# Optimization experiments

Hardware: AMD Instinct MI355X
Metric: run time of the kernel (lower is better)

The kernel has to match this reference:

```python
import jax, jax.numpy as jnp
import numpy as np

K = 3
PAD = 1
STRIDE = 1
DIL = 1


def _conv_offset(x, w, b):
    # standard 3x3 conv, NCHW
    out = jax.lax.conv_general_dilated(
        x, w, window_strides=(STRIDE, STRIDE), padding=((PAD, PAD), (PAD, PAD)),
        rhs_dilation=(DIL, DIL), dimension_numbers=('NCHW', 'OIHW', 'NCHW'))
    return out + b[None, :, None, None]


def _bilinear_sample(x, px, py):
    # x: (b,c,h,w); px,py: (b,N) absolute pixel coords; zero padding outside.
    b, c, h, w = x.shape
    x_flat = x.reshape(b, c, h * w)
    x0 = jnp.floor(px)
    y0 = jnp.floor(py)
    wx1 = px - x0
    wy1 = py - y0
    wx0 = 1.0 - wx1
    wy0 = 1.0 - wy1

    def gather(xi, yi, wt):
        valid = (xi >= 0) & (xi <= w - 1) & (yi >= 0) & (yi <= h - 1)
        xc = jnp.clip(xi, 0, w - 1).astype(jnp.int32)
        yc = jnp.clip(yi, 0, h - 1).astype(jnp.int32)
        idx = yc * w + xc  # (b,N)
        v = jax.vmap(lambda xf, i: jnp.take(xf, i, axis=1))(x_flat, idx)  # (b,c,N)
        return v * (wt * valid.astype(x.dtype))[:, None, :]

    out = gather(x0, y0, wy0 * wx0)
    out = out + gather(x0 + 1, y0, wy0 * wx1)
    out = out + gather(x0, y0 + 1, wy1 * wx0)
    out = out + gather(x0 + 1, y0 + 1, wy1 * wx1)
    return out


def setup_inputs() -> dict:
    key = jax.random.key(0)
    k1, k2, k3, k4 = jax.random.split(key, 4)
    x = jax.random.normal(k1, (8, 64, 128, 128), dtype=jnp.float32)
    # small random offset-predictor weights (repo inits to zero; random gives nonzero offsets)
    w_off = jax.random.normal(k2, (27, 64, 3, 3), dtype=jnp.float32) * 0.01
    b_off = jax.random.normal(k3, (27,), dtype=jnp.float32) * 0.01
    w_conv = jax.random.normal(k4, (64, 576), dtype=jnp.float32) / np.sqrt(3.0 * 576.0)
    return {"x": x, "w_off": w_off, "b_off": b_off, "w_conv": w_conv}


def reference(x, w_off, b_off, w_conv):
    b, c, h, w = x.shape
    out = _conv_offset(x, w_off, b_off)  # (b, 3*K*K, H, W)
    H, W = out.shape[2], out.shape[3]
    o1, o2, m = jnp.split(out, 3, axis=1)  # each (b, K*K, H, W)
    mask = jax.nn.sigmoid(m).reshape(b, 1, K, K, H, W)
    # base grid (absolute coords), per module __init__
    x_start = DIL / 2 * (K - 1) - PAD  # = 0.0 here
    y_start = DIL / 2 * (K - 1) - PAD
    x_cood = (x_start + STRIDE * jnp.arange(W)).astype(x.dtype)
    y_cood = (y_start + STRIDE * jnp.arange(H)).astype(x.dtype)
    # per-tap kernel bias, tap order is (kh, kw) row-major
    taps = (jnp.arange(K) - (K - 1) / 2) * DIL
    x_bias = jnp.tile(taps, K).astype(x.dtype)      # (K*K,)
    y_bias = jnp.repeat(taps, K).astype(x.dtype)    # (K*K,)
    px = o1 + x_cood[None, None, None, :] + x_bias[None, :, None, None]  # (b,9,H,W)
    py = o2 + y_cood[None, None, :, None] + y_bias[None, :, None, None]
    N = K * K * H * W
    y = _bilinear_sample(x, px.reshape(b, N), py.reshape(b, N))  # (b,c,N)
    y = y.reshape(b, c, K, K, H, W) * mask
    y = y.reshape(b, c * K * K, H, W)
    # 1x1 conv == channel GEMM
    return jnp.einsum('bkhw,ok->bohw', y, w_conv)
```

## Files before the change

### kernel.cpp

```cpp
#include <hip/hip_runtime.h>
#include <math.h>

#define HW_   128
#define CIN_  64
#define IMG_  (HW_ * HW_)

#define TR_    6
#define TC_    40
#define PIT_   36
#define TILEDW (TR_ * TC_ * PIT_)

typedef short    s16x8 __attribute__((ext_vector_type(8)));
typedef float    f32x4 __attribute__((ext_vector_type(4)));
typedef float    f32x2 __attribute__((ext_vector_type(2)));
typedef unsigned u32x4 __attribute__((ext_vector_type(4)));

__device__ __forceinline__ short f2bf(float f) {
  union { float f; unsigned i; } v; v.f = f;
  unsigned r = (v.i + 0x7fffu + ((v.i >> 16) & 1u)) >> 16;
  return (short)r;
}

#if defined(__has_builtin)
#if __has_builtin(__builtin_amdgcn_cvt_pk_bf16_f32)
#define HAVE_CVT_PK_BF16 1
#endif
#endif

__device__ __forceinline__ unsigned PK2(float a, float b) {
#ifdef HAVE_CVT_PK_BF16
  typedef __bf16 bf16x2_t __attribute__((ext_vector_type(2)));
  union { bf16x2_t v; unsigned u; } cv;
  cv.v = __builtin_amdgcn_cvt_pk_bf16_f32(a, b);
  return cv.u;
#else
  union { float f; unsigned u; } ua, ub; ua.f = a; ub.f = b;
  unsigned ra = ua.u + 0x7fffu + ((ua.u >> 16) & 1u);
  unsigned rb = ub.u + 0x7fffu + ((ub.u >> 16) & 1u);
  return __builtin_amdgcn_perm(rb, ra, 0x07060302u);
#endif
}

__device__ __forceinline__ f32x2 up2d(unsigned d) {
  union { unsigned u; float f; } lo, hi;
  lo.u = d << 16; hi.u = d;
  return (f32x2){lo.f, hi.f};
}


__global__ __launch_bounds__(256) void wprep(const float* __restrict__ w_off,
                                             const float* __restrict__ w_conv,
                                             short* __restrict__ wOf,
                                             short* __restrict__ wA) {
  int t = blockIdx.x * 256 + threadIdx.x;
  if (t < 36864) {
    int i = t & 7, o = (t >> 3) & 63, q = (t >> 9) & 3, ks = (t >> 11) & 1, j = t >> 12;
    int c = ks * 32 + q * 8 + i;
    wA[t] = f2bf(w_conv[o * 576 + c * 9 + j]);
  }
  if (t < 18432) {
    int i = t & 7, m = (t >> 3) & 31, q = (t >> 8) & 3, ks = (t >> 10) & 1, j = t >> 11;
    int c = ks * 32 + q * 8 + i;
    wOf[t] = (m < 27) ? f2bf(w_off[(m * 64 + c) * 9 + j]) : (short)0;
  }
}

__global__ __launch_bounds__(256)
__attribute__((amdgpu_waves_per_eu(4)))
void dfuse(const float* __restrict__ x,
           const short* __restrict__ wOf,
           const float* __restrict__ b_off,
           const short* __restrict__ wA,
           float* __restrict__ out) {
  __shared__ __align__(16) unsigned lds_[TILEDW];

  int bi  = blockIdx.x & 7;
  int tid = blockIdx.x >> 3;
  int h0  = (tid >> 2) << 1;
  int w0  = (tid & 3) << 5;
  int t   = threadIdx.x;
  int wv  = t >> 6, l = t & 63;
  int col = l & 15, q = l >> 4;
  int px_local = wv * 16 + col;
  int rl  = px_local >> 5;
  int cl  = px_local & 31;
  int h   = h0 + rl;
  int w   = w0 + cl;
  int p   = h * HW_ + w;

  const float* xB = x + (size_t)bi * (CIN_ * IMG_);

  for (int u = t; u < TR_ * 32 * 10; u += 256) {
    int cc = u % 10;
    int rc = u / 10;
    int cp = rc & 31;
    int r  = rc >> 5;
    int y  = h0 - 2 + r;
    int ys = min(max(y, 0), HW_ - 1);
    int xg0 = w0 - 4 + cc * 4;
    int xs  = min(max(xg0, 0), HW_ - 4);
    bool ok = (y >= 0) && (y < HW_) && (xg0 >= 0) && (xg0 < HW_);
    const float* s0 = xB + (2 * cp) * IMG_ + ys * HW_ + xs;
    float4 f0 = *(const float4*)s0;
    float4 f1 = *(const float4*)(s0 + IMG_);
    int sd = (r * TC_ + cc * 4) * PIT_ + cp;
    lds_[sd]            = ok ? PK2(f0.x, f1.x) : 0u;
    lds_[sd + PIT_]     = ok ? PK2(f0.y, f1.y) : 0u;
    lds_[sd + 2 * PIT_] = ok ? PK2(f0.z, f1.z) : 0u;
    lds_[sd + 3 * PIT_] = ok ? PK2(f0.w, f1.w) : 0u;
  }
  __syncthreads();

  float oall[32];
  {
    const short* wq = wOf + q * 256 + col * 8;
    f32x4 a0v = {0.f, 0.f, 0.f, 0.f};
    f32x4 a1v = {0.f, 0.f, 0.f, 0.f};
    const unsigned* tb = &lds_[((rl + 2) * TC_ + (cl + 4)) * PIT_ + q * 4];
#pragma unroll
    for (int j = 0; j < 9; ++j) {
      int dy = j / 3 - 1, dx = j % 3 - 1;
      const unsigned* tp = tb + (dy * TC_ + dx) * PIT_;
      union { u32x4 u; s16x8 v; } B0, B1;
      B0.u = *(const u32x4*)tp;
      B1.u = *(const u32x4*)(tp + 16);
      const short* wj = wq + j * 2048;
      s16x8 a00 = *(const s16x8*)(wj);
      s16x8 a01 = *(const s16x8*)(wj + 128);
      s16x8 a10 = *(const s16x8*)(wj + 1024);
      s16x8 a11 = *(const s16x8*)(wj + 1024 + 128);
      a0v = __builtin_amdgcn_mfma_f32_16x16x32_bf16(a00, B0.v, a0v, 0, 0, 0);
      a1v = __builtin_amdgcn_mfma_f32_16x16x32_bf16(a01, B0.v, a1v, 0, 0, 0);
      a0v = __builtin_amdgcn_mfma_f32_16x16x32_bf16(a10, B1.v, a0v, 0, 0, 0);
      a1v = __builtin_amdgcn_mfma_f32_16x16x32_bf16(a11, B1.v, a1v, 0, 0, 0);
    }
    float myv[8];
#pragma unroll
    for (int r = 0; r < 4; ++r) myv[r] = a0v[r] + b_off[q * 4 + r];
#pragma unroll
    for (int r = 0; r < 4; ++r) {
      int ch = 16 + q * 4 + r;
      float bo = b_off[min(ch, 26)];
      float v = a1v[r] + bo;
      myv[4 + r] = (ch >= 18) ? (1.f / (1.f + __expf(-v))) : v;
    }
#pragma unroll
    for (int qq = 0; qq < 4; ++qq) {
      int src = qq * 16 + col;
#pragma unroll
      for (int r = 0; r < 4; ++r) {
        oall[qq * 4 + r]      = __shfl(myv[r], src);
        oall[16 + qq * 4 + r] = __shfl(myv[4 + r], src);
      }
    }
  }

  f32x4 acc[4];
#pragma unroll
  for (int ms = 0; ms < 4; ++ms) acc[ms] = (f32x4){0.f, 0.f, 0.f, 0.f};

  const short* wqA = wA + q * 512 + col * 8;

#pragma unroll
  for (int j = 0; j < 9; ++j) {
    float o1 = oall[j], o2 = oall[9 + j], mk = oall[18 + j];

    float pxf = o1 + (float)(w + (j % 3) - 1);
    float pyf = o2 + (float)(h + (j / 3) - 1);
    float fx = floorf(pxf), fy = floorf(pyf);
    int   x0 = (int)fx,   y0 = (int)fy;
    float ax = pxf - fx, ay = pyf - fy;
    float bx = 1.f - ax, by = 1.f - ay;

    bx = (x0 >= 0  && x0 < HW_)     ? bx : 0.f;
    ax = (x0 >= -1 && x0 < HW_ - 1) ? ax : 0.f;
    by = (y0 >= 0  && y0 < HW_)     ? by : 0.f;
    ay = (y0 >= -1 && y0 < HW_ - 1) ? ay : 0.f;
    float bym = by * mk, aym = ay * mk;
    float u00 = bym * bx, u01 = bym * ax;
    float u10 = aym * bx, u11 = aym * ax;
    f32x2 U00 = {u00, u00}, U01 = {u01, u01};
    f32x2 U10 = {u10, u10}, U11 = {u11, u11};

    unsigned F0u[4], F1u[4];
    bool intile = (o1 >= -1.f) && (o1 < 1.f) && (o2 >= -1.f) && (o2 < 1.f);
    if (intile) {
      int r0 = y0 - (h0 - 2), c0 = x0 - (w0 - 4);
      const unsigned* t00 = &lds_[(r0 * TC_ + c0) * PIT_ + q * 4];
      u32x4 A00 = *(const u32x4*)(t00);
      u32x4 A01 = *(const u32x4*)(t00 + PIT_);
      u32x4 A10 = *(const u32x4*)(t00 + TC_ * PIT_);
      u32x4 A11 = *(const u32x4*)(t00 + TC_ * PIT_ + PIT_);
      u32x4 B00 = *(const u32x4*)(t00 + 16);
      u32x4 B01 = *(const u32x4*)(t00 + PIT_ + 16);
      u32x4 B10 = *(const u32x4*)(t00 + TC_ * PIT_ + 16);
      u32x4 B11 = *(const u32x4*)(t00 + TC_ * PIT_ + PIT_ + 16);
#pragma unroll
      for (int i = 0; i < 4; ++i) {
        f32x2 v0 = up2d(A00[i]) * U00 + up2d(A01[i]) * U01
                 + up2d(A10[i]) * U10 + up2d(A11[i]) * U11;
        F0u[i] = PK2(v0.x, v0.y);
        f32x2 v1 = up2d(B00[i]) * U00 + up2d(B01[i]) * U01
                 + up2d(B10[i]) * U10 + up2d(B11[i]) * U11;
        F1u[i] = PK2(v1.x, v1.y);
      }
    } else {
      int xc0 = min(max(x0, 0), HW_ - 1), xc1 = min(max(x0 + 1, 0), HW_ - 1);
      int yc0 = min(max(y0, 0), HW_ - 1), yc1 = min(max(y0 + 1, 0), HW_ - 1);
      int g00 = yc0 * HW_ + xc0, g01 = yc0 * HW_ + xc1;
      int g10 = yc1 * HW_ + xc0, g11 = yc1 * HW_ + xc1;
      for (int hB = 0; hB < 2; ++hB) {
        for (int ii = 0; ii < 4; ++ii) {
          int c0i = hB * 32 + q * 8 + 2 * ii;
          const float* pc = xB + c0i * IMG_;
          const float* pd = pc + IMG_;
          float va = u00 * pc[g00] + u01 * pc[g01] + u10 * pc[g10] + u11 * pc[g11];
          float vb = u00 * pd[g00] + u01 * pd[g01] + u10 * pd[g10] + u11 * pd[g11];
          if (hB) F1u[ii] = PK2(va, vb); else F0u[ii] = PK2(va, vb);
        }
      }
    }

    union { unsigned u[4]; s16x8 v; } F0, F1;
#pragma unroll
    for (int i = 0; i < 4; ++i) { F0.u[i] = F0u[i]; F1.u[i] = F1u[i]; }

    const short* wj = wqA + j * 4096;
#pragma unroll
    for (int ms = 0; ms < 4; ++ms) {
      s16x8 a0 = *(const s16x8*)(wj + ms * 128);
      acc[ms] = __builtin_amdgcn_mfma_f32_16x16x32_bf16(a0, F0.v, acc[ms], 0, 0, 0);
    }
#pragma unroll
    for (int ms = 0; ms < 4; ++ms) {
      s16x8 a1 = *(const s16x8*)(wj + 2048 + ms * 128);
      acc[ms] = __builtin_amdgcn_mfma_f32_16x16x32_bf16(a1, F1.v, acc[ms], 0, 0, 0);
    }
  }

  float* op = out + (size_t)bi * (CIN_ * IMG_) + p;
#pragma unroll
  for (int ms = 0; ms < 4; ++ms)
#pragma unroll
    for (int r = 0; r < 4; ++r)
      op[(ms * 16 + q * 4 + r) * IMG_] = acc[ms][r];
}

extern "C" void kernel_launch(void* const* d_in, const int* in_sizes, int n_in,
                              void* d_out, int out_size, void* d_ws, size_t ws_size,
                              hipStream_t stream) {
  const float* x      = (const float*)d_in[0];
  const float* w_off  = (const float*)d_in[1];
  const float* b_off  = (const float*)d_in[2];
  const float* w_conv = (const float*)d_in[3];
  float* out = (float*)d_out;

  char* ws = (char*)d_ws;
  short* wOf = (short*)(ws);
  short* wA  = (short*)(ws + 36864);

  hipLaunchKernelGGL(wprep, dim3(144),  dim3(256), 0, stream, w_off, w_conv, wOf, wA);
  hipLaunchKernelGGL(dfuse, dim3(2048), dim3(256), 0, stream, x, wOf, b_off, wA, out);
}
```

Baseline: 127.9 us.

## Pre-pack input to pixel-major bf16 layout with swizzled LDS tile

New measurement: 162.3 us. 26.9% more time.

```diff
diff --git a/kernel.cpp b/kernel.cpp
--- a/kernel.cpp
+++ b/kernel.cpp
@@ -7,8 +7,17 @@
 
 #define TR_    6
 #define TC_    40
-#define PIT_   36
+#define PIT_   32
 #define TILEDW (TR_ * TC_ * PIT_)
+
+#define OPIT_  36
+#define OTILE  (TR_ * TC_ * OPIT_)
+
+#define WOF_BYTES 36864
+#define WA_BYTES  73728
+#define XB_OFF    (WOF_BYTES + WA_BYTES)
+#define XB_DW     ((size_t)8 * IMG_ * 32)
+#define WS_NEED   (XB_OFF + (XB_DW + 32) * 4)
 
 typedef short    s16x8 __attribute__((ext_vector_type(8)));
 typedef float    f32x4 __attribute__((ext_vector_type(4)));
@@ -65,13 +74,47 @@
   }
 }
 
+__global__ __launch_bounds__(256) void xprep(const float* __restrict__ x,
+                                             unsigned* __restrict__ xb) {
+  __shared__ __align__(16) unsigned xl[128 * 36];
+  int bi  = blockIdx.x & 7;
+  int row = blockIdx.x >> 3;
+  int t   = threadIdx.x;
+  int cp  = t >> 3;
+  int wq  = t & 7;
+
+  const float* xRow = x + (size_t)bi * (CIN_ * IMG_) + row * HW_;
+  const float* s0 = xRow + (2 * cp) * IMG_;
+#pragma unroll
+  for (int k = 0; k < 4; ++k) {
+    float4 f0 = *(const float4*)(s0 + k * 32 + wq * 4);
+    float4 f1 = *(const float4*)(s0 + IMG_ + k * 32 + wq * 4);
+    int w = k * 32 + wq * 4;
+    xl[(w    ) * 36 + cp] = PK2(f0.x, f1.x);
+    xl[(w + 1) * 36 + cp] = PK2(f0.y, f1.y);
+    xl[(w + 2) * 36 + cp] = PK2(f0.z, f1.z);
+    xl[(w + 3) * 36 + cp] = PK2(f0.w, f1.w);
+  }
+  __syncthreads();
+
+  unsigned* xbI = xb + (size_t)bi * (IMG_ * 32) + (size_t)row * (HW_ * 32);
+#pragma unroll
+  for (int k = 0; k < 4; ++k) {
+    int i = t + k * 256;
+    int px = i >> 3, chunk = i & 7;
+    u32x4 v = *(const u32x4*)(xl + px * 36 + chunk * 4);
+    *(u32x4*)(xbI + (size_t)px * 32 + chunk * 4) = v;
+  }
+  if (blockIdx.x == 0 && t < 32) xb[XB_DW + t] = 0u;
+}
+
 __global__ __launch_bounds__(256)
-__attribute__((amdgpu_waves_per_eu(4)))
-void dfuse(const float* __restrict__ x,
-           const short* __restrict__ wOf,
-           const float* __restrict__ b_off,
-           const short* __restrict__ wA,
-           float* __restrict__ out) {
+__attribute__((amdgpu_waves_per_eu(5)))
+void dfuse2(const unsigned* __restrict__ xb,
+            const short* __restrict__ wOf,
+            const float* __restrict__ b_off,
+            const short* __restrict__ wA,
+            float* __restrict__ out) {
   __shared__ __align__(16) unsigned lds_[TILEDW];
 
   int bi  = blockIdx.x & 7;
@@ -88,6 +131,181 @@
   int w   = w0 + cl;
   int p   = h * HW_ + w;
 
+  const unsigned* xbB = xb + (size_t)bi * (IMG_ * 32);
+
+  for (int u = t; u < TR_ * TC_ * 8; u += 256) {
+    int chunk = u & 7, pxl = u >> 3;
+    int r = pxl / TC_, c = pxl % TC_;
+    int y  = h0 - 2 + r;
+    int ys = min(max(y, 0), HW_ - 1);
+    int xg = w0 - 4 + c;
+    int xs = min(max(xg, 0), HW_ - 1);
+    bool ok = (y >= 0) && (y < HW_) && (xg >= 0) && (xg < HW_);
+    u32x4 v = *(const u32x4*)(xbB + (size_t)(ys * HW_ + xs) * 32 + (chunk << 2));
+    if (!ok) v = (u32x4){0u, 0u, 0u, 0u};
+    *(u32x4*)(lds_ + pxl * PIT_ + ((chunk ^ (c & 7)) << 2)) = v;
+  }
+  __syncthreads();
+
+  float oall[32];
+  {
+    const short* wq_ = wOf + q * 256 + col * 8;
+    f32x4 a0v = {0.f, 0.f, 0.f, 0.f};
+    f32x4 a1v = {0.f, 0.f, 0.f, 0.f};
+    const unsigned* tbp = lds_ + ((rl + 2) * TC_ + (cl + 4)) * PIT_;
+#pragma unroll
+    for (int j = 0; j < 9; ++j) {
+      int dy = j / 3 - 1, dx = j % 3 - 1;
+      int ca = (q ^ ((cl + 4 + dx) & 7)) << 2;
+      const unsigned* pb = tbp + (dy * TC_ + dx) * PIT_;
+      union { u32x4 u; s16x8 v; } B0, B1;
+      B0.u = *(const u32x4*)(pb + ca);
+      B1.u = *(const u32x4*)(pb + (ca ^ 16));
+      const short* wj = wq_ + j * 2048;
+      s16x8 a00 = *(const s16x8*)(wj);
+      s16x8 a01 = *(const s16x8*)(wj + 128);
+      s16x8 a10 = *(const s16x8*)(wj + 1024);
+      s16x8 a11 = *(const s16x8*)(wj + 1024 + 128);
+      a0v = __builtin_amdgcn_mfma_f32_16x16x32_bf16(a00, B0.v, a0v, 0, 0, 0);
+      a1v = __builtin_amdgcn_mfma_f32_16x16x32_bf16(a01, B0.v, a1v, 0, 0, 0);
+      a0v = __builtin_amdgcn_mfma_f32_16x16x32_bf16(a10, B1.v, a0v, 0, 0, 0);
+      a1v = __builtin_amdgcn_mfma_f32_16x16x32_bf16(a11, B1.v, a1v, 0, 0, 0);
+    }
+    float myv[8];
+#pragma unroll
+    for (int r = 0; r < 4; ++r) myv[r] = a0v[r] + b_off[q * 4 + r];
+#pragma unroll
+    for (int r = 0; r < 4; ++r) {
+      int ch = 16 + q * 4 + r;
+      float bo = b_off[min(ch, 26)];
+      float v = a1v[r] + bo;
+      myv[4 + r] = (ch >= 18) ? (1.f / (1.f + __expf(-v))) : v;
+    }
+#pragma unroll
+    for (int qq = 0; qq < 4; ++qq) {
+      int src = qq * 16 + col;
+#pragma unroll
+      for (int r = 0; r < 4; ++r) {
+        oall[qq * 4 + r]      = __shfl(myv[r], src);
+        oall[16 + qq * 4 + r] = __shfl(myv[4 + r], src);
+      }
+    }
+  }
+
+  f32x4 acc[4];
+#pragma unroll
+  for (int ms = 0; ms < 4; ++ms) acc[ms] = (f32x4){0.f, 0.f, 0.f, 0.f};
+
+  const short* wqA = wA + q * 512 + col * 8;
+
+#pragma unroll
+  for (int j = 0; j < 9; ++j) {
+    float o1 = oall[j], o2 = oall[9 + j], mk = oall[18 + j];
+
+    float pxf = o1 + (float)(w + (j % 3) - 1);
+    float pyf = o2 + (float)(h + (j / 3) - 1);
+    float fx = floorf(pxf), fy = floorf(pyf);
+    int   x0 = (int)fx,   y0 = (int)fy;
+    float ax = pxf - fx, ay = pyf - fy;
+    float bx = 1.f - ax, by = 1.f - ay;
+
+    bx = (x0 >= 0  && x0 < HW_)     ? bx : 0.f;
+    ax = (x0 >= -1 && x0 < HW_ - 1) ? ax : 0.f;
+    by = (y0 >= 0  && y0 < HW_)     ? by : 0.f;
+    ay = (y0 >= -1 && y0 < HW_ - 1) ? ay : 0.f;
+    float bym = by * mk, aym = ay * mk;
+    float u00 = bym * bx, u01 = bym * ax;
+    float u10 = aym * bx, u11 = aym * ax;
+    f32x2 U00 = {u00, u00}, U01 = {u01, u01};
+    f32x2 U10 = {u10, u10}, U11 = {u11, u11};
+
+    u32x4 A00, A01, A10, A11, B00, B01, B10, B11;
+    bool intile = (o1 >= -1.f) && (o1 < 1.f) && (o2 >= -1.f) && (o2 < 1.f);
+    if (intile) {
+      int r0 = y0 - (h0 - 2), c0 = x0 - (w0 - 4);
+      const unsigned* b00 = lds_ + (r0 * TC_ + c0) * PIT_;
+      int s0 = (q ^ (c0 & 7)) << 2;
+      int s1 = (q ^ ((c0 + 1) & 7)) << 2;
+      A00 = *(const u32x4*)(b00 + s0);
+      A01 = *(const u32x4*)(b00 + PIT_ + s1);
+      A10 = *(const u32x4*)(b00 + TC_ * PIT_ + s0);
+      A11 = *(const u32x4*)(b00 + TC_ * PIT_ + PIT_ + s1);
+      B00 = *(const u32x4*)(b00 + (s0 ^ 16));
+      B01 = *(const u32x4*)(b00 + PIT_ + (s1 ^ 16));
+      B10 = *(const u32x4*)(b00 + TC_ * PIT_ + (s0 ^ 16));
+      B11 = *(const u32x4*)(b00 + TC_ * PIT_ + PIT_ + (s1 ^ 16));
+    } else {
+      int xc0 = min(max(x0, 0), HW_ - 1), xc1 = min(max(x0 + 1, 0), HW_ - 1);
+      int yc0 = min(max(y0, 0), HW_ - 1), yc1 = min(max(y0 + 1, 0), HW_ - 1);
+      const unsigned* g00 = xbB + (size_t)(yc0 * HW_ + xc0) * 32 + (q << 2);
+      const unsigned* g01 = xbB + (size_t)(yc0 * HW_ + xc1) * 32 + (q << 2);
+      const unsigned* g10 = xbB + (size_t)(yc1 * HW_ + xc0) * 32 + (q << 2);
+      const unsigned* g11 = xbB + (size_t)(yc1 * HW_ + xc1) * 32 + (q << 2);
+      A00 = *(const u32x4*)g00; B00 = *(const u32x4*)(g00 + 16);
+      A01 = *(const u32x4*)g01; B01 = *(const u32x4*)(g01 + 16);
+      A10 = *(const u32x4*)g10; B10 = *(const u32x4*)(g10 + 16);
+      A11 = *(const u32x4*)g11; B11 = *(const u32x4*)(g11 + 16);
+    }
+
+    unsigned F0u[4], F1u[4];
+#pragma unroll
+    for (int i = 0; i < 4; ++i) {
+      f32x2 v0 = up2d(A00[i]) * U00 + up2d(A01[i]) * U01
+               + up2d(A10[i]) * U10 + up2d(A11[i]) * U11;
+      F0u[i] = PK2(v0.x, v0.y);
+      f32x2 v1 = up2d(B00[i]) * U00 + up2d(B01[i]) * U01
+               + up2d(B10[i]) * U10 + up2d(B11[i]) * U11;
+      F1u[i] = PK2(v1.x, v1.y);
+    }
+
+    union { unsigned u[4]; s16x8 v; } F0, F1;
+#pragma unroll
+    for (int i = 0; i < 4; ++i) { F0.u[i] = F0u[i]; F1.u[i] = F1u[i]; }
+
+    const short* wj = wqA + j * 4096;
+#pragma unroll
+    for (int ms = 0; ms < 4; ++ms) {
+      s16x8 a0 = *(const s16x8*)(wj + ms * 128);
+      acc[ms] = __builtin_amdgcn_mfma_f32_16x16x32_bf16(a0, F0.v, acc[ms], 0, 0, 0);
+    }
+#pragma unroll
+    for (int ms = 0; ms < 4; ++ms) {
+      s16x8 a1 = *(const s16x8*)(wj + 2048 + ms * 128);
+      acc[ms] = __builtin_amdgcn_mfma_f32_16x16x32_bf16(a1, F1.v, acc[ms], 0, 0, 0);
+    }
+  }
+
+  float* op = out + (size_t)bi * (CIN_ * IMG_) + p;
+#pragma unroll
+  for (int ms = 0; ms < 4; ++ms)
+#pragma unroll
+    for (int r = 0; r < 4; ++r)
+      op[(ms * 16 + q * 4 + r) * IMG_] = acc[ms][r];
+}
+
+__global__ __launch_bounds__(256)
+__attribute__((amdgpu_waves_per_eu(4)))
+void dfuse_f32(const float* __restrict__ x,
+               const short* __restrict__ wOf,
+               const float* __restrict__ b_off,
+               const short* __restrict__ wA,
+               float* __restrict__ out) {
+  __shared__ __align__(16) unsigned lds_[OTILE];
+
+  int bi  = blockIdx.x & 7;
+  int tid = blockIdx.x >> 3;
+  int h0  = (tid >> 2) << 1;
+  int w0  = (tid & 3) << 5;
+  int t   = threadIdx.x;
+  int wv  = t >> 6, l = t & 63;
+  int col = l & 15, q = l >> 4;
+  int px_local = wv * 16 + col;
+  int rl  = px_local >> 5;
+  int cl  = px_local & 31;
+  int h   = h0 + rl;
+  int w   = w0 + cl;
+  int p   = h * HW_ + w;
+
   const float* xB = x + (size_t)bi * (CIN_ * IMG_);
 
   for (int u = t; u < TR_ * 32 * 10; u += 256) {
@@ -103,11 +321,11 @@
     const float* s0 = xB + (2 * cp) * IMG_ + ys * HW_ + xs;
     float4 f0 = *(const float4*)s0;
     float4 f1 = *(const float4*)(s0 + IMG_);
-    int sd = (r * TC_ + cc * 4) * PIT_ + cp;
-    lds_[sd]            = ok ? PK2(f0.x, f1.x) : 0u;
-    lds_[sd + PIT_]     = ok ? PK2(f0.y, f1.y) : 0u;
-    lds_[sd + 2 * PIT_] = ok ? PK2(f0.z, f1.z) : 0u;
-    lds_[sd + 3 * PIT_] = ok ? PK2(f0.w, f1.w) : 0u;
+    int sd = (r * TC_ + cc * 4) * OPIT_ + cp;
+    lds_[sd]             = ok ? PK2(f0.x, f1.x) : 0u;
+    lds_[sd + OPIT_]     = ok ? PK2(f0.y, f1.y) : 0u;
+    lds_[sd + 2 * OPIT_] = ok ? PK2(f0.z, f1.z) : 0u;
+    lds_[sd + 3 * OPIT_] = ok ? PK2(f0.w, f1.w) : 0u;
   }
   __syncthreads();
 
@@ -116,11 +334,11 @@
     const short* wq = wOf + q * 256 + col * 8;
     f32x4 a0v = {0.f, 0.f, 0.f, 0.f};
     f32x4 a1v = {0.f, 0.f, 0.f, 0.f};
-    const unsigned* tb = &lds_[((rl + 2) * TC_ + (cl + 4)) * PIT_ + q * 4];
+    const unsigned* tb = &lds_[((rl + 2) * TC_ + (cl + 4)) * OPIT_ + q * 4];
 #pragma unroll
     for (int j = 0; j < 9; ++j) {
       int dy = j / 3 - 1, dx = j % 3 - 1;
-      const unsigned* tp = tb + (dy * TC_ + dx) * PIT_;
+      const unsigned* tp = tb + (dy * TC_ + dx) * OPIT_;
       union { u32x4 u; s16x8 v; } B0, B1;
       B0.u = *(const u32x4*)tp;
       B1.u = *(const u32x4*)(tp + 16);
@@ -186,15 +404,15 @@
     bool intile = (o1 >= -1.f) && (o1 < 1.f) && (o2 >= -1.f) && (o2 < 1.f);
     if (intile) {
       int r0 = y0 - (h0 - 2), c0 = x0 - (w0 - 4);
-      const unsigned* t00 = &lds_[(r0 * TC_ + c0) * PIT_ + q * 4];
+      const unsigned* t00 = &lds_[(r0 * TC_ + c0) * OPIT_ + q * 4];
       u32x4 A00 = *(const u32x4*)(t00);
-      u32x4 A01 = *(const u32x4*)(t00 + PIT_);
-      u32x4 A10 = *(const u32x4*)(t00 + TC_ * PIT_);
-      u32x4 A11 = *(const u32x4*)(t00 + TC_ * PIT_ + PIT_);
+      u32x4 A01 = *(const u32x4*)(t00 + OPIT_);
+      u32x4 A10 = *(const u32x4*)(t00 + TC_ * OPIT_);
+      u32x4 A11 = *(const u32x4*)(t00 + TC_ * OPIT_ + OPIT_);
       u32x4 B00 = *(const u32x4*)(t00 + 16);
-      u32x4 B01 = *(const u32x4*)(t00 + PIT_ + 16);
-      u32x4 B10 = *(const u32x4*)(t00 + TC_ * PIT_ + 16);
-      u32x4 B11 = *(const u32x4*)(t00 + TC_ * PIT_ + PIT_ + 16);
+      u32x4 B01 = *(const u32x4*)(t00 + OPIT_ + 16);
+      u32x4 B10 = *(const u32x4*)(t00 + TC_ * OPIT_ + 16);
+      u32x4 B11 = *(const u32x4*)(t00 + TC_ * OPIT_ + OPIT_ + 16);
 #pragma unroll
       for (int i = 0; i < 4; ++i) {
         f32x2 v0 = up2d(A00[i]) * U00 + up2d(A01[i]) * U01
@@ -257,8 +475,15 @@
 
   char* ws = (char*)d_ws;
   short* wOf = (short*)(ws);
-  short* wA  = (short*)(ws + 36864);
-
-  hipLaunchKernelGGL(wprep, dim3(144),  dim3(256), 0, stream, w_off, w_conv, wOf, wA);
-  hipLaunchKernelGGL(dfuse, dim3(2048), dim3(256), 0, stream, x, wOf, b_off, wA, out);
-}
+  short* wA  = (short*)(ws + WOF_BYTES);
+
+  hipLaunchKernelGGL(wprep, dim3(144), dim3(256), 0, stream, w_off, w_conv, wOf, wA);
+
+  if (ws_size >= WS_NEED) {
+    unsigned* xb = (unsigned*)(ws + XB_OFF);
+    hipLaunchKernelGGL(xprep,  dim3(1024), dim3(256), 0, stream, x, xb);
+    hipLaunchKernelGGL(dfuse2, dim3(2048), dim3(256), 0, stream, xb, wOf, b_off, wA, out);
+  } else {
+    hipLaunchKernelGGL(dfuse_f32, dim3(2048), dim3(256), 0, stream, x, wOf, b_off, wA, out);
+  }
+}
```
